# Performance work log

Hardware: AMD Instinct MI355X
Metric: run time of the kernel (lower is better)

The kernel has to match this reference:

```python
import jax, jax.numpy as jnp
import numpy as np

B, C, T, W, H = 4, 128, 16, 64, 64


def setup_inputs() -> dict:
    key = jax.random.key(0)
    ks = jax.random.split(key, 5)
    Cq = C // 8
    return {
        "x": jax.random.normal(ks[0], (B, C, T, W, H), jnp.float32),
        # stacked params for the 3 cells (T, W, H order, as in nn.Sequential)
        "Wq": jax.random.normal(ks[1], (3, Cq, C), jnp.float32) * 0.05,
        "bq": jnp.zeros((3, Cq), jnp.float32),
        "Wk": jax.random.normal(ks[2], (3, Cq, C), jnp.float32) * 0.05,
        "bk": jnp.zeros((3, Cq), jnp.float32),
        "Wv": jax.random.normal(ks[3], (3, C, C), jnp.float32) * 0.05,
        "bv": jnp.zeros((3, C), jnp.float32),
        # gamma is init to 0 in torch (identity); small random so the test is nontrivial
        "gamma": jax.random.normal(ks[4], (3,), jnp.float32) * 0.1,
    }


def _conv1x1(x, w, b):
    # 1x1x1 Conv3d == channel contraction
    return jnp.einsum('bcthw,oc->bothw', x, w) + b[None, :, None, None, None]


def _cell(x, wq, bq, wk, bk, wv, bv, gamma, attn_dim):
    # Faithful to torch: raw contiguous .view() == row-major reshape.
    Bb, Cc, Tt, Ww, Hh = x.shape
    q = _conv1x1(x, wq, bq).reshape(Bb, attn_dim, -1)   # (B, A, N)
    k = _conv1x1(x, wk, bk).reshape(Bb, -1, attn_dim)   # (B, N, A)  (pooling_factor=1 -> MaxPool identity)
    attn = jax.nn.softmax(jnp.matmul(q, k), axis=-1)    # (B, A, A)
    v = _conv1x1(x, wv, bv).reshape(Bb, -1, attn_dim)   # (B, M, A), M = C*T*W*H/A
    out = jnp.matmul(v, attn.swapaxes(1, 2))            # (B, M, A)
    out = out.reshape(Bb, Cc, Ww, Hh, Tt).transpose(0, 1, 4, 2, 3)  # -> (B, C, T, W, H)
    return gamma * out + x


def reference(x, Wq, bq, Wk, bk, Wv, bv, gamma):
    _, _, Tt, Ww, Hh = x.shape
    attn_dims = (Tt, Ww, Hh)  # cells with attn_id 'T', 'W', 'H'
    for i in range(3):
        x = _cell(x, Wq[i], bq[i], Wk[i], bk[i], Wv[i], bv[i], gamma[i], attn_dims[i])
    return x
```

## Files before the change

kernel.cpp:

```cpp
#include <hip/hip_runtime.h>

#define BB 4
#define CC 128
#define CQ 16
#define TDIM 16
#define SS 65536
#define CS (CC*SS)
#define NBLK 256

typedef unsigned short u16;
typedef unsigned int   u32;

typedef __bf16 bf16x8v __attribute__((ext_vector_type(8)));
typedef float  floatx4v __attribute__((ext_vector_type(4)));

__device__ __forceinline__ u16 f2bf(float f) {
    u32 u = __float_as_uint(f);
    u32 r = (u + 0x7fffu + ((u >> 16) & 1u)) >> 16;
    return (u16)r;
}
__device__ __forceinline__ void unpack8(uint4 r, float* f) {
    f[0] = __uint_as_float(r.x << 16); f[1] = __uint_as_float(r.x & 0xffff0000u);
    f[2] = __uint_as_float(r.y << 16); f[3] = __uint_as_float(r.y & 0xffff0000u);
    f[4] = __uint_as_float(r.z << 16); f[5] = __uint_as_float(r.z & 0xffff0000u);
    f[6] = __uint_as_float(r.w << 16); f[7] = __uint_as_float(r.w & 0xffff0000u);
}
__device__ __forceinline__ bf16x8v ld_bf8(const void* p) {
    union { uint4 u; bf16x8v b; } x;
    x.u = *(const uint4*)p;
    return x.b;
}

__global__ __launch_bounds__(256) void wconv_kernel(
    const float* __restrict__ Wq, const float* __restrict__ Wk, const float* __restrict__ Wv,
    const float* __restrict__ bq, const float* __restrict__ bk, const float* __restrict__ bv,
    u16* __restrict__ wbf, float* __restrict__ bias)
{
    const int idx = blockIdx.x * 256 + threadIdx.x;
    const int cell = idx / 20480;
    const int j = idx - cell * 20480;
    const int o = j >> 7, c = j & 127;
    float v;
    if (o < 16)      v = Wq[(cell * 16 + o) * 128 + c];
    else if (o < 32) v = Wk[(cell * 16 + (o - 16)) * 128 + c];
    else             v = Wv[(cell * 128 + (o - 32)) * 128 + c];
    wbf[idx] = f2bf(v);
    if (idx < 480) {
        const int cl = idx / 160, oo = idx - cl * 160;
        float b = (oo < 16) ? bq[cl * 16 + oo]
                : (oo < 32) ? bk[cl * 16 + oo - 16]
                :             bv[cl * 128 + oo - 32];
        bias[idx] = b;
    }
}

__global__ __launch_bounds__(512, 4) void qkv_mfma_kernel(
    const float* __restrict__ x,
    const u16* __restrict__ wbf, const float* __restrict__ bias,
    float* __restrict__ qf, float* __restrict__ kf, u16* __restrict__ vf)
{
    __shared__ u16 xT[128 * 128];
    const int t  = threadIdx.x;
    const int b  = blockIdx.y;
    const int s0 = blockIdx.x << 7;
    const float* xb = x + (size_t)b * CS;

    {
        const int sl = t & 127;
        const int cb = (t >> 7) << 3;
        const float* xs = xb + s0 + sl;
        const u32 rowb = (u32)sl << 8;
        const u32 swz  = (u32)(sl & 7) << 4;
#pragma unroll
        for (int p = 0; p < 4; p++) {
            const int c0 = p * 32 + cb;
            float f[8];
#pragma unroll
            for (int j = 0; j < 8; j++) f[j] = xs[(size_t)(c0 + j) * SS];
            uint4 pk;
            pk.x = (u32)f2bf(f[0]) | ((u32)f2bf(f[1]) << 16);
            pk.y = (u32)f2bf(f[2]) | ((u32)f2bf(f[3]) << 16);
            pk.z = (u32)f2bf(f[4]) | ((u32)f2bf(f[5]) << 16);
            pk.w = (u32)f2bf(f[6]) | ((u32)f2bf(f[7]) << 16);
            *(uint4*)((char*)xT + ((rowb + (u32)(c0 << 1)) ^ swz)) = pk;
        }
    }
    __syncthreads();

    const int lane = t & 63;
    const int wv   = t >> 6;
    const int mh   = wv >> 2;
    const int sq   = wv & 3;
    const int ln15 = lane & 15;
    const int lhi  = lane >> 4;

    floatx4v acc[5][2] = {};

    const u16* abase = wbf + ((mh * 80 + ln15) << 7) + (lhi << 3);
    const u32 swzB = (u32)(ln15 & 7) << 4;
    const int sbase = sq * 32 + ln15;

#pragma unroll
    for (int ks = 0; ks < 4; ks++) {
        bf16x8v af[5];
#pragma unroll
        for (int mi = 0; mi < 5; mi++)
            af[mi] = ld_bf8(abase + (mi << 11) + (ks << 5));
#pragma unroll
        for (int nt = 0; nt < 2; nt++) {
            const u32 off = (((u32)(sbase + nt * 16) << 8)
                           + (u32)((ks << 6) + (lhi << 4))) ^ swzB;
            bf16x8v bf = ld_bf8((const char*)xT + off);
#pragma unroll
            for (int mi = 0; mi < 5; mi++)
                acc[mi][nt] = __builtin_amdgcn_mfma_f32_16x16x32_bf16(
                                  af[mi], bf, acc[mi][nt], 0, 0, 0);
        }
    }

    float* qb = qf + (size_t)b * ((size_t)CQ * SS);
    float* kb = kf + (size_t)b * ((size_t)CQ * SS);
    u16*   vb = vf + (size_t)b * (size_t)CS;

#pragma unroll
    for (int mi = 0; mi < 5; mi++) {
        const int o0 = mh * 80 + mi * 16 + lhi * 4;
        float bia[4];
        *(float4*)bia = *(const float4*)(bias + o0);
#pragma unroll
        for (int nt = 0; nt < 2; nt++) {
            const int s = s0 + sq * 32 + nt * 16 + ln15;
            if (o0 < 16) {
#pragma unroll
                for (int r = 0; r < 4; r++)
                    qb[(size_t)(o0 + r) * SS + s] = acc[mi][nt][r] + bia[r];
            } else if (o0 < 32) {
#pragma unroll
                for (int r = 0; r < 4; r++)
                    kb[(size_t)(o0 - 16 + r) * SS + s] = acc[mi][nt][r] + bia[r];
            } else {
#pragma unroll
                for (int r = 0; r < 4; r++)
                    vb[(size_t)(o0 - 32 + r) * SS + s] = f2bf(acc[mi][nt][r] + bia[r]);
            }
        }
    }
}

template <int A>
__global__ __launch_bounds__(256) void logits_part_kernel(
    const float* __restrict__ qf, const float* __restrict__ kf,
    float* __restrict__ part)
{
    constexpr int N = (CQ * SS) / A;
    constexpr int NCHUNK = N / NBLK;
    constexpr int NLOG = (NCHUNK == 64) ? 6 : 8;
    __shared__ float qs[A][NCHUNK + 1];
    __shared__ float ks[NCHUNK][A];
    const int t  = threadIdx.x;
    const int b  = blockIdx.y;
    const int n0 = blockIdx.x << NLOG;
    const float* qb = qf + (size_t)b * ((size_t)CQ * SS);
    const float* kb = kf + (size_t)b * ((size_t)CQ * SS);

    for (int idx = t; idx < A * NCHUNK; idx += 256) {
        int a1 = idx >> NLOG, n = idx & (NCHUNK - 1);
        qs[a1][n] = qb[(size_t)a1 * N + n0 + n];
    }
    float* ksf = &ks[0][0];
    for (int idx = t; idx < NCHUNK * A; idx += 256)
        ksf[idx] = kb[(size_t)n0 * A + idx];
    __syncthreads();

    float* pb = part + ((size_t)b * NBLK + blockIdx.x) * (A * A);

    if constexpr (A == 16) {
        int a1 = t >> 4, a2 = t & 15;
        float s = 0.f;
#pragma unroll 8
        for (int n = 0; n < NCHUNK; n++) s += qs[a1][n] * ks[n][a2];
        pb[t] = s;
    } else {
        int a1  = t & 63;
        int a2b = (t >> 6) * 16;
        float acc[16];
#pragma unroll
        for (int j = 0; j < 16; j++) acc[j] = 0.f;
        for (int n = 0; n < NCHUNK; n++) {
            float q = qs[a1][n];
#pragma unroll
            for (int j = 0; j < 16; j++) acc[j] += q * ks[n][a2b + j];
        }
        float* dst = pb + t * 16;
        *(float4*)(dst)      = make_float4(acc[0],  acc[1],  acc[2],  acc[3]);
        *(float4*)(dst + 4)  = make_float4(acc[4],  acc[5],  acc[6],  acc[7]);
        *(float4*)(dst + 8)  = make_float4(acc[8],  acc[9],  acc[10], acc[11]);
        *(float4*)(dst + 12) = make_float4(acc[12], acc[13], acc[14], acc[15]);
    }
}

template <int A>
__global__ __launch_bounds__(256) void reduce_softmax_kernel(
    const float* __restrict__ part, float* __restrict__ attn, u16* __restrict__ pbf)
{
    constexpr int NG = 256 / A;
    __shared__ float red[NG][A];
    const int a1 = blockIdx.x;
    const int b  = blockIdx.y;
    const int t  = threadIdx.x;
    const int a2 = t & (A - 1);
    const int g  = t >> ((A == 16) ? 4 : 6);
    const float* pb = part + (size_t)b * NBLK * (A * A);

    int off;
    if constexpr (A == 16) off = a1 * 16 + a2;
    else                   off = a1 * 16 + ((a2 >> 4) << 10) + (a2 & 15);

    float s0 = 0.f, s1 = 0.f, s2 = 0.f, s3 = 0.f;
    for (int blk = g; blk < NBLK; blk += 4 * NG) {
        s0 += pb[(size_t)(blk         ) * (A * A) + off];
        s1 += pb[(size_t)(blk +     NG) * (A * A) + off];
        s2 += pb[(size_t)(blk + 2 * NG) * (A * A) + off];
        s3 += pb[(size_t)(blk + 3 * NG) * (A * A) + off];
    }
    red[g][a2] = (s0 + s1) + (s2 + s3);
    __syncthreads();

    if (t < A) {
        float l = 0.f;
#pragma unroll
        for (int gg = 0; gg < NG; gg++) l += red[gg][t];
        float m = l;
#pragma unroll
        for (int o2 = A / 2; o2 > 0; o2 >>= 1) m = fmaxf(m, __shfl_xor(m, o2, 64));
        float e = expf(l - m);
        float s = e;
#pragma unroll
        for (int o2 = A / 2; o2 > 0; o2 >>= 1) s += __shfl_xor(s, o2, 64);
        const float p = e / s;
        attn[((size_t)b << 12) + a1 * A + t] = p;
        if constexpr (A == 64)
            pbf[((size_t)b << 12) + a1 * 64 + t] = f2bf(p);
    }
}

__global__ __launch_bounds__(256) void out16_kernel(
    const float* __restrict__ x, const u16* __restrict__ vf,
    const float* __restrict__ attn, const float* __restrict__ gptr,
    float* __restrict__ y)
{
    const int b = blockIdx.y;
    const u32 u = blockIdx.x * 256u + threadIdx.x;
    const float g = *gptr;
    const float* ab = attn + ((size_t)b << 12);
    const float* xb = x + (size_t)b * CS;
    float*       yb = y + (size_t)b * CS;
    const u16*   vr = vf + (size_t)b * CS + (size_t)u * 16;

    uint4 r0 = *(const uint4*)(vr);
    uint4 r1 = *(const uint4*)(vr + 8);
    float v0[8], v1[8];
    unpack8(r0, v0); unpack8(r1, v1);

    const size_t base = ((size_t)(u >> 12) << 16) + (u & 4095u);
#pragma unroll
    for (int tt = 0; tt < 16; tt++) {
        const float* ar = ab + tt * 16;
        float4 a0 = *(const float4*)(ar);
        float4 a1 = *(const float4*)(ar + 4);
        float4 a2 = *(const float4*)(ar + 8);
        float4 a3 = *(const float4*)(ar + 12);
        float acc = v0[0]*a0.x + v0[1]*a0.y + v0[2]*a0.z + v0[3]*a0.w
                  + v0[4]*a1.x + v0[5]*a1.y + v0[6]*a1.z + v0[7]*a1.w
                  + v1[0]*a2.x + v1[1]*a2.y + v1[2]*a2.z + v1[3]*a2.w
                  + v1[4]*a3.x + v1[5]*a3.y + v1[6]*a3.z + v1[7]*a3.w;
        const size_t i = base + ((size_t)tt << 12);
        yb[i] = g * acc + xb[i];
    }
}

__global__ __launch_bounds__(256) void out64_mfma_kernel(
    const float* __restrict__ x, const u16* __restrict__ vf,
    const u16* __restrict__ pbf, const float* __restrict__ gptr,
    float* __restrict__ y)
{
    const int b = blockIdx.y;
    const int t = threadIdx.x;
    const float g = *gptr;
    const int lane = t & 63;
    const int ln15 = lane & 15;
    const int lhi  = lane >> 4;
    const int wv   = t >> 6;
    const int m0w  = blockIdx.x * 256 + wv * 64;

    const u16*   pb = pbf + ((size_t)b << 12);
    const u16*   vb = vf + (size_t)b * CS;
    const float* xb = x + (size_t)b * CS;
    float*       yb = y + (size_t)b * CS;

    bf16x8v af[2][4];
#pragma unroll
    for (int ksi = 0; ksi < 2; ksi++)
#pragma unroll
        for (int sub = 0; sub < 4; sub++)
            af[ksi][sub] = ld_bf8(pb + (sub * 16 + ln15) * 64 + ksi * 32 + lhi * 8);

#pragma unroll
    for (int tile = 0; tile < 4; tile++) {
        const int m0 = m0w + tile * 16;
        const u16* vrow = vb + ((size_t)(m0 + ln15) << 6) + (lhi << 3);
        bf16x8v b0 = ld_bf8(vrow);
        bf16x8v b1 = ld_bf8(vrow + 32);

        floatx4v acc[4] = {};
#pragma unroll
        for (int sub = 0; sub < 4; sub++) {
            acc[sub] = __builtin_amdgcn_mfma_f32_16x16x32_bf16(af[0][sub], b0, acc[sub], 0, 0, 0);
            acc[sub] = __builtin_amdgcn_mfma_f32_16x16x32_bf16(af[1][sub], b1, acc[sub], 0, 0, 0);
        }

        const int c   = m0 >> 10;
        const int ow  = ((m0 >> 6) & 15) * 4 + ((m0 & 63) >> 4);
        const size_t base = ((size_t)c << 16) + ((size_t)ow << 6) + (size_t)(ln15 << 2);
        const float* xbase = xb + base;
        float*       ybase = yb + base;
#pragma unroll
        for (int r = 0; r < 4; r++) {
            const int ot = lhi * 4 + r;
            float4 xv = *(const float4*)(xbase + ((size_t)ot << 12));
            float4 o;
            o.x = g * acc[0][r] + xv.x;
            o.y = g * acc[1][r] + xv.y;
            o.z = g * acc[2][r] + xv.z;
            o.w = g * acc[3][r] + xv.w;
            *(float4*)(ybase + ((size_t)ot << 12)) = o;
        }
    }
}

extern "C" void kernel_launch(void* const* d_in, const int* in_sizes, int n_in,
                              void* d_out, int out_size, void* d_ws, size_t ws_size,
                              hipStream_t stream)
{
    (void)in_sizes; (void)n_in; (void)out_size;
    const float* x0    = (const float*)d_in[0];
    const float* Wq    = (const float*)d_in[1];
    const float* bq    = (const float*)d_in[2];
    const float* Wk    = (const float*)d_in[3];
    const float* bk    = (const float*)d_in[4];
    const float* Wv    = (const float*)d_in[5];
    const float* bv    = (const float*)d_in[6];
    const float* gamma = (const float*)d_in[7];
    float* y = (float*)d_out;

    const size_t MiB = (size_t)1 << 20;
    const size_t need4 = 4 * (28 * MiB + 16384 + 8192) + 160 * 128 * 3 * 2 + 3 * 160 * 4;
    const int nb = (ws_size >= need4) ? 4 : 1;

    char* ws = (char*)d_ws;
    float* qf    = (float*)ws;
    float* kf    = (float*)(ws + (size_t)nb * 4  * MiB);
    u16*   vf    = (u16*)  (ws + (size_t)nb * 8  * MiB);
    float* part  = (float*)(ws + (size_t)nb * 24 * MiB);
    float* attnp = (float*)(ws + (size_t)nb * 28 * MiB);
    u16*   pbf   = (u16*)  (ws + (size_t)nb * 28 * MiB + (size_t)nb * 16384);
    u16*   wbf3  = (u16*)  (ws + (size_t)nb * 28 * MiB + (size_t)nb * (16384 + 8192));
    float* bias3 = (float*)(ws + (size_t)nb * 28 * MiB + (size_t)nb * (16384 + 8192)
                               + 160 * 128 * 3 * 2);

    wconv_kernel<<<240, 256, 0, stream>>>(Wq, Wk, Wv, bq, bk, bv, wbf3, bias3);

    for (int cell = 0; cell < 3; cell++) {
        const u16*   wc = wbf3  + (size_t)cell * 160 * 128;
        const float* bc = bias3 + (size_t)cell * 160;
        for (int b0 = 0; b0 < BB; b0 += nb) {
            const float* xin = ((cell == 0) ? x0 : (const float*)y) + (size_t)b0 * CS;
            float* yb = y + (size_t)b0 * CS;

            qkv_mfma_kernel<<<dim3(512, nb), 512, 0, stream>>>(xin, wc, bc, qf, kf, vf);

            if (cell == 0) {
                logits_part_kernel<16><<<dim3(NBLK, nb), 256, 0, stream>>>(qf, kf, part);
                reduce_softmax_kernel<16><<<dim3(16, nb), 256, 0, stream>>>(part, attnp, pbf);
                out16_kernel<<<dim3(2048, nb), 256, 0, stream>>>(xin, vf, attnp, gamma + cell, yb);
            } else {
                logits_part_kernel<64><<<dim3(NBLK, nb), 256, 0, stream>>>(qf, kf, part);
                reduce_softmax_kernel<64><<<dim3(64, nb), 256, 0, stream>>>(part, attnp, pbf);
                out64_mfma_kernel<<<dim3(512, nb), 256, 0, stream>>>(xin, vf, pbf, gamma + cell, yb);
            }
        }
    }
}
```

Baseline: 630.1 us.

## Vectorize x loads and stage V output through LDS for coalesced stores

The x tile load now uses float4 reads along the spatial dimension and scatters bf16 values into a transposed, XOR-swizzled LDS tile, instead of scalar strided reads. The V output is first written into LDS in channel-major order, then stored to global memory with 16-byte coalesced writes rather than scattered 2-byte stores. This targets global memory transaction efficiency on both the input and output sides. The cost is extra LDS traffic, scalar 2-byte LDS writes with possible bank conflicts, and two more block barriers.

```diff
diff --git a/kernel.cpp b/kernel.cpp
--- a/kernel.cpp
+++ b/kernel.cpp
@@ -66,23 +66,20 @@
     const float* xb = x + (size_t)b * CS;
 
     {
-        const int sl = t & 127;
-        const int cb = (t >> 7) << 3;
-        const float* xs = xb + s0 + sl;
-        const u32 rowb = (u32)sl << 8;
-        const u32 swz  = (u32)(sl & 7) << 4;
-#pragma unroll
-        for (int p = 0; p < 4; p++) {
-            const int c0 = p * 32 + cb;
-            float f[8];
-#pragma unroll
-            for (int j = 0; j < 8; j++) f[j] = xs[(size_t)(c0 + j) * SS];
-            uint4 pk;
-            pk.x = (u32)f2bf(f[0]) | ((u32)f2bf(f[1]) << 16);
-            pk.y = (u32)f2bf(f[2]) | ((u32)f2bf(f[3]) << 16);
-            pk.z = (u32)f2bf(f[4]) | ((u32)f2bf(f[5]) << 16);
-            pk.w = (u32)f2bf(f[6]) | ((u32)f2bf(f[7]) << 16);
-            *(uint4*)((char*)xT + ((rowb + (u32)(c0 << 1)) ^ swz)) = pk;
+        const int s4 = (t & 31) << 2;
+        const int cr = t >> 5;
+        const float* xs = xb + s0 + s4;
+#pragma unroll
+        for (int p = 0; p < 8; p++) {
+            const int c = cr + p * 16;
+            float4 f = *(const float4*)(xs + (size_t)c * SS);
+            u16 h[4] = { f2bf(f.x), f2bf(f.y), f2bf(f.z), f2bf(f.w) };
+#pragma unroll
+            for (int j = 0; j < 4; j++) {
+                const int sl = s4 + j;
+                const u32 sw = (u32)(((sl & 7) ^ ((sl >> 3) & 7)) << 4);
+                *(u16*)((char*)xT + ((((u32)sl << 8) + ((u32)c << 1)) ^ sw)) = h[j];
+            }
         }
     }
     __syncthreads();
@@ -97,8 +94,6 @@
     floatx4v acc[5][2] = {};
 
     const u16* abase = wbf + ((mh * 80 + ln15) << 7) + (lhi << 3);
-    const u32 swzB = (u32)(ln15 & 7) << 4;
-    const int sbase = sq * 32 + ln15;
 
 #pragma unroll
     for (int ks = 0; ks < 4; ks++) {
@@ -108,8 +103,9 @@
             af[mi] = ld_bf8(abase + (mi << 11) + (ks << 5));
 #pragma unroll
         for (int nt = 0; nt < 2; nt++) {
-            const u32 off = (((u32)(sbase + nt * 16) << 8)
-                           + (u32)((ks << 6) + (lhi << 4))) ^ swzB;
+            const int sl = sq * 32 + nt * 16 + ln15;
+            const u32 sw = (u32)(((sl & 7) ^ ((sl >> 3) & 7)) << 4);
+            const u32 off = (((u32)sl << 8) + (u32)((ks << 6) + (lhi << 4))) ^ sw;
             bf16x8v bf = ld_bf8((const char*)xT + off);
 #pragma unroll
             for (int mi = 0; mi < 5; mi++)
@@ -122,28 +118,54 @@
     float* kb = kf + (size_t)b * ((size_t)CQ * SS);
     u16*   vb = vf + (size_t)b * (size_t)CS;
 
+    if (mh == 0) {
+#pragma unroll
+        for (int mi = 0; mi < 2; mi++) {
+            const int o0 = mi * 16 + lhi * 4;
+            float bia[4];
+            *(float4*)bia = *(const float4*)(bias + o0);
+            float* base = (mi == 0) ? qb : kb;
+            const int row0 = o0 & 15;
+#pragma unroll
+            for (int nt = 0; nt < 2; nt++) {
+                const int s = s0 + sq * 32 + nt * 16 + ln15;
+#pragma unroll
+                for (int r = 0; r < 4; r++)
+                    base[(size_t)(row0 + r) * SS + s] = acc[mi][nt][r] + bia[r];
+            }
+        }
+    }
+    __syncthreads();
+
 #pragma unroll
     for (int mi = 0; mi < 5; mi++) {
         const int o0 = mh * 80 + mi * 16 + lhi * 4;
-        float bia[4];
-        *(float4*)bia = *(const float4*)(bias + o0);
-#pragma unroll
-        for (int nt = 0; nt < 2; nt++) {
-            const int s = s0 + sq * 32 + nt * 16 + ln15;
-            if (o0 < 16) {
-#pragma unroll
-                for (int r = 0; r < 4; r++)
-                    qb[(size_t)(o0 + r) * SS + s] = acc[mi][nt][r] + bia[r];
-            } else if (o0 < 32) {
-#pragma unroll
-                for (int r = 0; r < 4; r++)
-                    kb[(size_t)(o0 - 16 + r) * SS + s] = acc[mi][nt][r] + bia[r];
-            } else {
-#pragma unroll
-                for (int r = 0; r < 4; r++)
-                    vb[(size_t)(o0 - 32 + r) * SS + s] = f2bf(acc[mi][nt][r] + bia[r]);
+        if (o0 >= 32) {
+            float bia[4];
+            *(float4*)bia = *(const float4*)(bias + o0);
+            const int vc0 = o0 - 32;
+#pragma unroll
+            for (int nt = 0; nt < 2; nt++) {
+                const int sl = sq * 32 + nt * 16 + ln15;
+#pragma unroll
+                for (int r = 0; r < 4; r++) {
+                    const int vc = vc0 + r;
+                    const u32 sw = (u32)(((vc & 7) ^ ((vc >> 3) & 7)) << 4);
+                    *(u16*)((char*)xT + ((((u32)vc << 8) + ((u32)sl << 1)) ^ sw))
+                        = f2bf(acc[mi][nt][r] + bia[r]);
+                }
             }
         }
+    }
+    __syncthreads();
+
+#pragma unroll
+    for (int it = 0; it < 4; it++) {
+        const int vc = (t >> 4) + it * 32;
+        const u32 sw = (u32)(((vc & 7) ^ ((vc >> 3) & 7)) << 4);
+        uint4 d = *(const uint4*)((char*)xT +
+                      ((((u32)vc << 8) + ((u32)(t & 15) << 4)) ^ sw));
+        *(uint4*)(vb + (size_t)vc * SS + s0 + ((t & 15) << 3)) = d;
     }
 }
 
```

Result: no change. 626.9 us (-0.5%).
